# Kernel optimization log

Hardware: AMD Instinct MI355X
Metric: run time of the kernel (lower is better)

## Reference

```python
import jax, jax.numpy as jnp
import numpy as np

B, N, D_IN, D_OUT, H = 64, 512, 256, 256, 4
HD = D_OUT // H


def setup_inputs() -> dict:
    key = jax.random.key(0)
    ks = jax.random.split(key, 10)
    x = jax.random.normal(ks[0], (B, N, D_IN), dtype=jnp.float32)
    adj = jax.random.randint(ks[1], (N, N), 0, 2, dtype=jnp.int32)
    adj = adj.at[jnp.arange(N), jnp.arange(N)].set(1)  # self-loops: no empty rows
    s_in = 1.0 / np.sqrt(D_IN)
    s_out = 1.0 / np.sqrt(D_OUT)
    wq = jax.random.uniform(ks[2], (D_OUT, D_IN), jnp.float32, -s_in, s_in)
    bq = jax.random.uniform(ks[3], (D_OUT,), jnp.float32, -s_in, s_in)
    wk = jax.random.uniform(ks[4], (D_OUT, D_IN), jnp.float32, -s_in, s_in)
    bk = jax.random.uniform(ks[5], (D_OUT,), jnp.float32, -s_in, s_in)
    wv = jax.random.uniform(ks[6], (D_OUT, D_IN), jnp.float32, -s_in, s_in)
    bv = jax.random.uniform(ks[7], (D_OUT,), jnp.float32, -s_in, s_in)
    wo = jax.random.uniform(ks[8], (D_OUT, D_OUT), jnp.float32, -s_out, s_out)
    bo = jax.random.uniform(ks[9], (D_OUT,), jnp.float32, -s_out, s_out)
    return {"x": x, "adj": adj, "wq": wq, "bq": bq, "wk": wk, "bk": bk,
            "wv": wv, "bv": bv, "wo": wo, "bo": bo}


def reference(x, adj, wq, bq, wk, bk, wv, bv, wo, bo):
    b, n, _ = x.shape
    # [B,N,D_out] -> [B,H,N,HD]
    q = (x @ wq.T + bq).reshape(b, n, H, HD).transpose(0, 2, 1, 3)
    k = (x @ wk.T + bk).reshape(b, n, H, HD).transpose(0, 2, 1, 3)
    v = (x @ wv.T + bv).reshape(b, n, H, HD).transpose(0, 2, 1, 3)
    scores = jnp.einsum('bhnd,bhmd->bhnm', q, k) / jnp.sqrt(jnp.float32(HD))
    scores = jnp.where(adj[None, None] == 0, -jnp.inf, scores)
    attn = jnp.nan_to_num(jax.nn.softmax(scores, axis=-1), nan=0.0)
    out = jnp.einsum('bhnm,bhmd->bhnd', attn, v)
    out = out.transpose(0, 2, 1, 3).reshape(b, n, D_OUT)
    return out @ wo.T + bo
```

## Files before the change

### kernel.cpp

```cpp
#include <hip/hip_runtime.h>
#include <stdint.h>

typedef float f32x4 __attribute__((ext_vector_type(4)));
typedef short s16x8 __attribute__((ext_vector_type(8)));
typedef unsigned short u16x4 __attribute__((ext_vector_type(4)));

#define BB 64
#define NN 512
#define DIN 256
#define DOUT 256
#define HH 4
#define HD 64

__device__ __forceinline__ unsigned short f2b(float f) {
  union { float f; unsigned u; } v; v.f = f;
  unsigned r = v.u + 0x7fffu + ((v.u >> 16) & 1u);
  return (unsigned short)(r >> 16);
}
__device__ __forceinline__ void mfma16(f32x4& acc, s16x8 a, s16x8 b) {
  acc = __builtin_amdgcn_mfma_f32_16x16x32_bf16(a, b, acc, 0, 0, 0);
}
__device__ __forceinline__ unsigned cvtpk(float lo, float hi) {
  unsigned r;
  asm("v_cvt_pk_bf16_f32 %0, %1, %2" : "=v"(r) : "v"(lo), "v"(hi));
  return r;
}

__global__ void k_conv(const float* __restrict__ src, unsigned short* __restrict__ dst, int n4) {
  int i = blockIdx.x * blockDim.x + threadIdx.x;
  if (i >= n4) return;
  f32x4 v = ((const f32x4*)src)[i];
  u16x4 o;
  o[0] = f2b(v[0]); o[1] = f2b(v[1]); o[2] = f2b(v[2]); o[3] = f2b(v[3]);
  ((u16x4*)dst)[i] = o;
}

__global__ void k_adjbits(const int* __restrict__ adj, unsigned long long* __restrict__ ab) {
  int row = blockIdx.x;
  int w = threadIdx.x >> 6, lane = threadIdx.x & 63;
  int v = adj[row * NN + w * 64 + lane];
  unsigned long long m = __ballot(v != 0);
  if (lane == 0) ab[row * 8 + w] = m;
}

__global__ __launch_bounds__(256) void k_qkv(
    const unsigned short* __restrict__ xh,
    const unsigned short* __restrict__ wqh,
    const unsigned short* __restrict__ wkh,
    const unsigned short* __restrict__ wvh,
    const float* __restrict__ bq, const float* __restrict__ bk, const float* __restrict__ bv,
    unsigned short* __restrict__ Qb, unsigned short* __restrict__ Kb, unsigned short* __restrict__ Vtb)
{
  __shared__ __align__(16) unsigned char xs[32768];
  __shared__ __align__(16) unsigned char wsl[32768];
  int tid = threadIdx.x, wave = tid >> 6, lane = tid & 63;
  int lr = lane & 15, lk = lane >> 4;
  int t0 = blockIdx.x * 64;
  int by = blockIdx.y, seg = by >> 2, nb0 = (by & 3) * 64;
  const unsigned short* wh = seg == 0 ? wqh : (seg == 1 ? wkh : wvh);
  const float* bias = seg == 0 ? bq : (seg == 1 ? bk : bv);
  int h = by & 3;

  const unsigned short* xsrc = xh + (size_t)t0 * DIN;
  const unsigned short* wsrc = wh + (size_t)nb0 * DIN;
#pragma unroll
  for (int i = 0; i < 8; ++i) {
    int lin = i * 256 + tid;
    int r = lin >> 5, c = lin & 31;
    int dst = r * 512 + ((c ^ (r & 7)) << 4);
    *(s16x8*)(xs + dst)  = *(const s16x8*)(xsrc + lin * 8);
    *(s16x8*)(wsl + dst) = *(const s16x8*)(wsrc + lin * 8);
  }
  __syncthreads();

  f32x4 acc[4] = {};
  if (seg < 2) {
    int chrow = wave * 16 + lr;
#pragma unroll
    for (int k0 = 0; k0 < 8; ++k0) {
      int cg = k0 * 4 + lk;
      s16x8 a = *(const s16x8*)(wsl + chrow * 512 + ((cg ^ (chrow & 7)) << 4));
#pragma unroll
      for (int ct = 0; ct < 4; ++ct) {
        int tr = ct * 16 + lr;
        s16x8 b = *(const s16x8*)(xs + tr * 512 + ((cg ^ (tr & 7)) << 4));
        mfma16(acc[ct], a, b);
      }
    }
    unsigned short* dst = (seg == 0) ? Qb : Kb;
    f32x4 bv4 = *(const f32x4*)(bias + nb0 + wave * 16 + lk * 4);
#pragma unroll
    for (int ct = 0; ct < 4; ++ct) {
      int n_ = t0 + ct * 16 + lr;
      int b_ = n_ >> 9, nn = n_ & 511;
      u16x4 pk;
#pragma unroll
      for (int j = 0; j < 4; ++j) pk[j] = f2b(acc[ct][j] + bv4[j]);
      *(u16x4*)(dst + ((size_t)(b_ * HH + h) * NN + nn) * HD + wave * 16 + lk * 4) = pk;
    }
  } else {
    int tokrow = wave * 16 + lr;
#pragma unroll
    for (int k0 = 0; k0 < 8; ++k0) {
      int cg = k0 * 4 + lk;
      s16x8 a = *(const s16x8*)(xs + tokrow * 512 + ((cg ^ (tokrow & 7)) << 4));
#pragma unroll
      for (int nt = 0; nt < 4; ++nt) {
        int cr = nt * 16 + lr;
        s16x8 b = *(const s16x8*)(wsl + cr * 512 + ((cg ^ (cr & 7)) << 4));
        mfma16(acc[nt], a, b);
      }
    }
    int m0 = t0 + wave * 16 + lk * 4;
    int b_ = m0 >> 9, n0 = m0 & 511;
#pragma unroll
    for (int nt = 0; nt < 4; ++nt) {
      int hd = nt * 16 + lr;
      float bs = bias[nb0 + hd];
      u16x4 pk;
#pragma unroll
      for (int j = 0; j < 4; ++j) pk[j] = f2b(acc[nt][j] + bs);
      *(u16x4*)(Vtb + ((size_t)(b_ * HH + h) * HD + hd) * NN + n0) = pk;
    }
  }
}

__global__ __launch_bounds__(512, 4) void k_attn(
    const unsigned short* __restrict__ Qb, const unsigned short* __restrict__ Kb,
    const unsigned short* __restrict__ Vtb, const unsigned long long* __restrict__ ab,
    unsigned short* __restrict__ att)
{
  __shared__ __align__(16) unsigned char kl[8192];
  __shared__ __align__(16) unsigned char vtl[8192];
  __shared__ __align__(16) unsigned char plb[32768];

  int tid = threadIdx.x, wave = tid >> 6, lane = tid & 63;
  int lr = lane & 15, lk = lane >> 4;
  int bid = blockIdx.x;
  int g = bid >> 4, r = bid & 15;
  int bh = g * 8 + (r & 7);
  int qt = r >> 3;
  int h = bh & 3, b_ = bh >> 2;
  const unsigned short* Qp = Qb + (size_t)bh * NN * HD;
  const unsigned short* Kp = Kb + (size_t)bh * NN * HD;
  const unsigned short* Vp = Vtb + (size_t)bh * HD * NN;
  int q0 = qt * 256 + wave * 32;

  s16x8 qa[2][2];
#pragma unroll
  for (int s = 0; s < 2; ++s) {
    qa[s][0] = *(const s16x8*)(Qp + (q0 + s * 16 + lr) * HD + lk * 8);
    qa[s][1] = *(const s16x8*)(Qp + (q0 + s * 16 + lr) * HD + 32 + lk * 8);
  }

  f32x4 oacc[2][4] = {};
  float rs[2] = {0.f, 0.f};
  unsigned char* plw = plb + wave * 4096;
  int sw = (lr & 7) << 4;

  int srow = tid >> 3, scol = tid & 7;
  int sdst = srow * 128 + ((scol * 16) ^ ((srow & 7) << 4));

  for (int kt = 0; kt < 8; ++kt) {
    *(s16x8*)(kl + sdst)  = *(const s16x8*)(Kp + (kt * 64 + srow) * HD + scol * 8);
    *(s16x8*)(vtl + sdst) = *(const s16x8*)(Vp + srow * NN + kt * 64 + scol * 8);
    unsigned long long abr[2];
#pragma unroll
    for (int s = 0; s < 2; ++s) abr[s] = ab[(size_t)(q0 + s * 16 + lr) * 8 + kt];
    __syncthreads();

#pragma unroll
    for (int s = 0; s < 2; ++s) {
#pragma unroll
      for (int ks = 0; ks < 4; ++ks) {
        int key = ks * 16 + lr;
        s16x8 kb0 = *(const s16x8*)(kl + key * 128 + ((lk * 16) ^ ((key & 7) << 4)));
        s16x8 kb1 = *(const s16x8*)(kl + key * 128 + ((64 + lk * 16) ^ ((key & 7) << 4)));
        f32x4 sx = {};
        mfma16(sx, kb0, qa[s][0]);
        mfma16(sx, kb1, qa[s][1]);
        float p[4];
#pragma unroll
        for (int j = 0; j < 4; ++j)
          p[j] = ((abr[s] >> (ks * 16 + lk * 4 + j)) & 1ULL) ? __expf(sx[j] * 0.125f) : 0.0f;
        unsigned w0 = cvtpk(p[0], p[1]);
        unsigned w1 = cvtpk(p[2], p[3]);
        union { unsigned u; float f; } t0, t1, t2, t3;
        t0.u = w0 << 16; t1.u = w0 & 0xffff0000u;
        t2.u = w1 << 16; t3.u = w1 & 0xffff0000u;
        rs[s] += (t0.f + t1.f) + (t2.f + t3.f);
        uint2 pw; pw.x = w0; pw.y = w1;
        *(uint2*)(plw + s * 2048 + lr * 128 + ((ks * 32 + lk * 8) ^ sw)) = pw;
      }
    }
#pragma unroll
    for (int s = 0; s < 2; ++s) {
      s16x8 pa0 = *(const s16x8*)(plw + s * 2048 + lr * 128 + ((lk * 16) ^ sw));
      s16x8 pa1 = *(const s16x8*)(plw + s * 2048 + lr * 128 + ((64 + lk * 16) ^ sw));
#pragma unroll
      for (int dt = 0; dt < 4; ++dt) {
        int d = dt * 16 + lr;
        s16x8 vb0 = *(const s16x8*)(vtl + d * 128 + ((lk * 16) ^ ((d & 7) << 4)));
        s16x8 vb1 = *(const s16x8*)(vtl + d * 128 + ((64 + lk * 16) ^ ((d & 7) << 4)));
        mfma16(oacc[s][dt], vb0, pa0);
        mfma16(oacc[s][dt], vb1, pa1);
      }
    }
    __syncthreads();
  }

#pragma unroll
  for (int s = 0; s < 2; ++s) {
    float v = rs[s];
    v += __shfl_xor(v, 16);
    v += __shfl_xor(v, 32);
    float rinv = 1.0f / v;
    int n_ = q0 + s * 16 + lr;
#pragma unroll
    for (int dt = 0; dt < 4; ++dt) {
      uint2 ow;
      ow.x = cvtpk(oacc[s][dt][0] * rinv, oacc[s][dt][1] * rinv);
      ow.y = cvtpk(oacc[s][dt][2] * rinv, oacc[s][dt][3] * rinv);
      *(uint2*)(att + ((size_t)(b_ * NN + n_) * DOUT) + h * HD + dt * 16 + lk * 4) = ow;
    }
  }
}

__global__ __launch_bounds__(256) void k_out(
    const unsigned short* __restrict__ att, const unsigned short* __restrict__ woh,
    const float* __restrict__ bo, float* __restrict__ out)
{
  __shared__ __align__(16) unsigned char as_[32768];
  __shared__ __align__(16) unsigned char wsl[32768];
  int tid = threadIdx.x, wave = tid >> 6, lane = tid & 63;
  int lr = lane & 15, lk = lane >> 4;
  int t0 = blockIdx.x * 64;
  int nb0 = blockIdx.y * 64;

  const unsigned short* asrc = att + (size_t)t0 * DOUT;
  const unsigned short* wsrc = woh + (size_t)nb0 * DOUT;
#pragma unroll
  for (int i = 0; i < 8; ++i) {
    int lin = i * 256 + tid;
    int r = lin >> 5, c = lin & 31;
    int dst = r * 512 + ((c ^ (r & 7)) << 4);
    *(s16x8*)(as_ + dst) = *(const s16x8*)(asrc + lin * 8);
    *(s16x8*)(wsl + dst) = *(const s16x8*)(wsrc + lin * 8);
  }
  __syncthreads();

  f32x4 acc[4] = {};
  int chrow = wave * 16 + lr;
#pragma unroll
  for (int k0 = 0; k0 < 8; ++k0) {
    int cg = k0 * 4 + lk;
    s16x8 a = *(const s16x8*)(wsl + chrow * 512 + ((cg ^ (chrow & 7)) << 4));
#pragma unroll
    for (int ct = 0; ct < 4; ++ct) {
      int tr = ct * 16 + lr;
      s16x8 b = *(const s16x8*)(as_ + tr * 512 + ((cg ^ (tr & 7)) << 4));
      mfma16(acc[ct], a, b);
    }
  }
  f32x4 bv4 = *(const f32x4*)(bo + nb0 + wave * 16 + lk * 4);
#pragma unroll
  for (int ct = 0; ct < 4; ++ct) {
    int m = t0 + ct * 16 + lr;
    f32x4 o = acc[ct] + bv4;
    *(f32x4*)(out + (size_t)m * DOUT + nb0 + wave * 16 + lk * 4) = o;
  }
}

extern "C" void kernel_launch(void* const* d_in, const int* in_sizes, int n_in,
                              void* d_out, int out_size, void* d_ws, size_t ws_size,
                              hipStream_t stream) {
  const float* x  = (const float*)d_in[0];
  const int*   adj = (const int*)d_in[1];
  const float* wq = (const float*)d_in[2];
  const float* bq = (const float*)d_in[3];
  const float* wk = (const float*)d_in[4];
  const float* bk = (const float*)d_in[5];
  const float* wv = (const float*)d_in[6];
  const float* bv = (const float*)d_in[7];
  const float* wo = (const float*)d_in[8];
  const float* bo = (const float*)d_in[9];
  float* out = (float*)d_out;

  char* ws = (char*)d_ws;
  size_t off = 0;
  auto carve = [&](size_t bytes) -> char* {
    off = (off + 255) & ~(size_t)255;
    char* p = ws + off;
    off += bytes;
    return p;
  };
  unsigned short* xh   = (unsigned short*)carve((size_t)BB * NN * DIN * 2);
  unsigned short* wqh  = (unsigned short*)carve((size_t)DOUT * DIN * 2);
  unsigned short* wkh  = (unsigned short*)carve((size_t)DOUT * DIN * 2);
  unsigned short* wvh  = (unsigned short*)carve((size_t)DOUT * DIN * 2);
  unsigned short* woh  = (unsigned short*)carve((size_t)DOUT * DOUT * 2);
  unsigned long long* abits = (unsigned long long*)carve((size_t)NN * 8 * 8);
  unsigned short* Qb   = (unsigned short*)carve((size_t)BB * HH * NN * HD * 2);
  unsigned short* Kb   = (unsigned short*)carve((size_t)BB * HH * NN * HD * 2);
  unsigned short* Vtb  = (unsigned short*)carve((size_t)BB * HH * HD * NN * 2);
  unsigned short* attb = (unsigned short*)carve((size_t)BB * NN * DOUT * 2);

  k_conv<<<dim3(8192), 256, 0, stream>>>(x, xh, (BB * NN * DIN) / 4);
  k_conv<<<dim3(64), 256, 0, stream>>>(wq, wqh, (DOUT * DIN) / 4);
  k_conv<<<dim3(64), 256, 0, stream>>>(wk, wkh, (DOUT * DIN) / 4);
  k_conv<<<dim3(64), 256, 0, stream>>>(wv, wvh, (DOUT * DIN) / 4);
  k_conv<<<dim3(64), 256, 0, stream>>>(wo, woh, (DOUT * DOUT) / 4);
  k_adjbits<<<dim3(512), 512, 0, stream>>>(adj, abits);
  k_qkv<<<dim3(512, 12), 256, 0, stream>>>(xh, wqh, wkh, wvh, bq, bk, bv, Qb, Kb, Vtb);
  k_attn<<<dim3(512), 512, 0, stream>>>(Qb, Kb, Vtb, abits, attb);
  k_out<<<dim3(512, 4), 256, 0, stream>>>(attb, woh, bo, out);
}
```

Measured before the change: 210.7 us.

## Double-buffer K/V tiles in attention and remap GEMM blocks for XCD locality

The attention kernel now double-buffers the K and V^T shared-memory tiles. It prefetches the next tile into registers while the current one is computed, which removes one barrier per iteration and hides global load latency. The QKV and output projection kernels switch to a 1D grid. Block indices are remapped so that all column tiles of one row tile land on the same XCD, improving L2 reuse of the x and attention rows. The cost is twice the K/V LDS footprint in the attention kernel, which may reduce occupancy, plus extra registers for the prefetched data.

```diff
diff --git a/kernel.cpp b/kernel.cpp
--- a/kernel.cpp
+++ b/kernel.cpp
@@ -55,19 +55,23 @@
   __shared__ __align__(16) unsigned char wsl[32768];
   int tid = threadIdx.x, wave = tid >> 6, lane = tid & 63;
   int lr = lane & 15, lk = lane >> 4;
-  int t0 = blockIdx.x * 64;
-  int by = blockIdx.y, seg = by >> 2, nb0 = (by & 3) * 64;
+  int bid = blockIdx.x;
+  int xcd = bid & 7, rest = bid >> 3;
+  int c = rest % 12;
+  int t = xcd + 8 * (rest / 12);
+  int t0 = t * 64;
+  int seg = c >> 2, nb0 = (c & 3) * 64;
   const unsigned short* wh = seg == 0 ? wqh : (seg == 1 ? wkh : wvh);
   const float* bias = seg == 0 ? bq : (seg == 1 ? bk : bv);
-  int h = by & 3;
+  int h = c & 3;
 
   const unsigned short* xsrc = xh + (size_t)t0 * DIN;
   const unsigned short* wsrc = wh + (size_t)nb0 * DIN;
 #pragma unroll
   for (int i = 0; i < 8; ++i) {
     int lin = i * 256 + tid;
-    int r = lin >> 5, c = lin & 31;
-    int dst = r * 512 + ((c ^ (r & 7)) << 4);
+    int r = lin >> 5, cc = lin & 31;
+    int dst = r * 512 + ((cc ^ (r & 7)) << 4);
     *(s16x8*)(xs + dst)  = *(const s16x8*)(xsrc + lin * 8);
     *(s16x8*)(wsl + dst) = *(const s16x8*)(wsrc + lin * 8);
   }
@@ -130,8 +134,8 @@
     const unsigned short* __restrict__ Vtb, const unsigned long long* __restrict__ ab,
     unsigned short* __restrict__ att)
 {
-  __shared__ __align__(16) unsigned char kl[8192];
-  __shared__ __align__(16) unsigned char vtl[8192];
+  __shared__ __align__(16) unsigned char kl[2][8192];
+  __shared__ __align__(16) unsigned char vtl[2][8192];
   __shared__ __align__(16) unsigned char plb[32768];
 
   int tid = threadIdx.x, wave = tid >> 6, lane = tid & 63;
@@ -160,22 +164,33 @@
 
   int srow = tid >> 3, scol = tid & 7;
   int sdst = srow * 128 + ((scol * 16) ^ ((srow & 7) << 4));
-
+  const unsigned short* ksrc = Kp + srow * HD + scol * 8;
+  const unsigned short* vsrc = Vp + srow * NN + scol * 8;
+
+  *(s16x8*)(kl[0] + sdst)  = *(const s16x8*)ksrc;
+  *(s16x8*)(vtl[0] + sdst) = *(const s16x8*)vsrc;
+  __syncthreads();
+
+#pragma unroll
   for (int kt = 0; kt < 8; ++kt) {
-    *(s16x8*)(kl + sdst)  = *(const s16x8*)(Kp + (kt * 64 + srow) * HD + scol * 8);
-    *(s16x8*)(vtl + sdst) = *(const s16x8*)(Vp + srow * NN + kt * 64 + scol * 8);
+    unsigned char* klc = kl[kt & 1];
+    unsigned char* vtc = vtl[kt & 1];
+    s16x8 gk, gv;
+    if (kt < 7) {
+      gk = *(const s16x8*)(ksrc + (kt + 1) * 64 * HD);
+      gv = *(const s16x8*)(vsrc + (kt + 1) * 64);
+    }
     unsigned long long abr[2];
 #pragma unroll
     for (int s = 0; s < 2; ++s) abr[s] = ab[(size_t)(q0 + s * 16 + lr) * 8 + kt];
-    __syncthreads();
 
 #pragma unroll
     for (int s = 0; s < 2; ++s) {
 #pragma unroll
       for (int ks = 0; ks < 4; ++ks) {
         int key = ks * 16 + lr;
-        s16x8 kb0 = *(const s16x8*)(kl + key * 128 + ((lk * 16) ^ ((key & 7) << 4)));
-        s16x8 kb1 = *(const s16x8*)(kl + key * 128 + ((64 + lk * 16) ^ ((key & 7) << 4)));
+        s16x8 kb0 = *(const s16x8*)(klc + key * 128 + ((lk * 16) ^ ((key & 7) << 4)));
+        s16x8 kb1 = *(const s16x8*)(klc + key * 128 + ((64 + lk * 16) ^ ((key & 7) << 4)));
         f32x4 sx = {};
         mfma16(sx, kb0, qa[s][0]);
         mfma16(sx, kb1, qa[s][1]);
@@ -200,13 +215,17 @@
 #pragma unroll
       for (int dt = 0; dt < 4; ++dt) {
         int d = dt * 16 + lr;
-        s16x8 vb0 = *(const s16x8*)(vtl + d * 128 + ((lk * 16) ^ ((d & 7) << 4)));
-        s16x8 vb1 = *(const s16x8*)(vtl + d * 128 + ((64 + lk * 16) ^ ((d & 7) << 4)));
+        s16x8 vb0 = *(const s16x8*)(vtc + d * 128 + ((lk * 16) ^ ((d & 7) << 4)));
+        s16x8 vb1 = *(const s16x8*)(vtc + d * 128 + ((64 + lk * 16) ^ ((d & 7) << 4)));
         mfma16(oacc[s][dt], vb0, pa0);
         mfma16(oacc[s][dt], vb1, pa1);
       }
     }
-    __syncthreads();
+    if (kt < 7) {
+      *(s16x8*)(kl[(kt & 1) ^ 1] + sdst)  = gk;
+      *(s16x8*)(vtl[(kt & 1) ^ 1] + sdst) = gv;
+      __syncthreads();
+    }
   }
 
 #pragma unroll
@@ -234,16 +253,20 @@
   __shared__ __align__(16) unsigned char wsl[32768];
   int tid = threadIdx.x, wave = tid >> 6, lane = tid & 63;
   int lr = lane & 15, lk = lane >> 4;
-  int t0 = blockIdx.x * 64;
-  int nb0 = blockIdx.y * 64;
+  int bid = blockIdx.x;
+  int xcd = bid & 7, rest = bid >> 3;
+  int c = rest & 3;
+  int t = xcd + 8 * (rest >> 2);
+  int t0 = t * 64;
+  int nb0 = c * 64;
 
   const unsigned short* asrc = att + (size_t)t0 * DOUT;
   const unsigned short* wsrc = woh + (size_t)nb0 * DOUT;
 #pragma unroll
   for (int i = 0; i < 8; ++i) {
     int lin = i * 256 + tid;
-    int r = lin >> 5, c = lin & 31;
-    int dst = r * 512 + ((c ^ (r & 7)) << 4);
+    int r = lin >> 5, cc = lin & 31;
+    int dst = r * 512 + ((cc ^ (r & 7)) << 4);
     *(s16x8*)(as_ + dst) = *(const s16x8*)(asrc + lin * 8);
     *(s16x8*)(wsl + dst) = *(const s16x8*)(wsrc + lin * 8);
   }
@@ -311,7 +334,7 @@
   k_conv<<<dim3(64), 256, 0, stream>>>(wv, wvh, (DOUT * DIN) / 4);
   k_conv<<<dim3(64), 256, 0, stream>>>(wo, woh, (DOUT * DOUT) / 4);
   k_adjbits<<<dim3(512), 512, 0, stream>>>(adj, abits);
-  k_qkv<<<dim3(512, 12), 256, 0, stream>>>(xh, wqh, wkh, wvh, bq, bk, bv, Qb, Kb, Vtb);
+  k_qkv<<<dim3(6144), 256, 0, stream>>>(xh, wqh, wkh, wvh, bq, bk, bv, Qb, Kb, Vtb);
   k_attn<<<dim3(512), 512, 0, stream>>>(Qb, Kb, Vtb, abits, attb);
-  k_out<<<dim3(512, 4), 256, 0, stream>>>(attb, woh, bo, out);
-}
+  k_out<<<dim3(2048), 256, 0, stream>>>(attb, woh, bo, out);
+}
```

After: 258.8 us. +22.8%, slower.
